# Kernel optimization log

Measured on AMD Instinct MI355X. Metric: run time of the kernel, lower is better.

## Reference

```python
import jax, jax.numpy as jnp
import numpy as np

B, S, ENC, DEC = 32, 4096, 512, 512

def setup_inputs() -> dict:
    key = jax.random.key(0)
    k1, k2, k3, k4 = jax.random.split(key, 4)
    encoder_outputs = jax.random.normal(k1, (B, S, ENC), dtype=jnp.float32)
    hidden = jax.random.normal(k2, (B, DEC), dtype=jnp.float32)
    # nn.Linear(enc+dec, 1): weight [1, enc+dec], bias [1]
    bound = 1.0 / np.sqrt(ENC + DEC)
    W = jax.random.uniform(k3, (1, ENC + DEC), minval=-bound, maxval=bound, dtype=jnp.float32)
    b = jax.random.uniform(k4, (1,), minval=-bound, maxval=bound, dtype=jnp.float32)
    return {"encoder_outputs": encoder_outputs, "hidden": hidden, "W": W, "b": b}

def reference(encoder_outputs, hidden, W, b):
    enc_dim = encoder_outputs.shape[-1]
    w_enc = W[0, :enc_dim]   # [enc]
    w_dec = W[0, enc_dim:]   # [dec]
    # energy = Linear(concat(enc, hidden_repeated)) == enc @ w_enc + hid @ w_dec + b
    energy = jnp.einsum('bse,e->bs', encoder_outputs, w_enc) \
           + (hidden @ w_dec)[:, None] + b[0]               # [B,S]
    weights = jax.nn.softmax(energy, axis=1)                 # [B,S]
    context = jnp.einsum('bs,bse->be', weights, encoder_outputs)  # [B,enc]
    return context
```

## Files before the change

### kernel.cpp

```cpp
#include <hip/hip_runtime.h>
#include <math.h>


#define B_ 32
#define S_ 4096
#define ENC_ 512
#define TPB 256
#define G 8

__device__ __forceinline__ float dot4(const float4 a, const float4 b) {
    return a.x * b.x + a.y * b.y + a.z * b.z + a.w * b.w;
}

__global__ __launch_bounds__(TPB) void attn_partial(
    const float* __restrict__ enc,
    const float* __restrict__ W,
    float* __restrict__ pm,
    float* __restrict__ pl,
    float* __restrict__ pc,
    int R, int P)
{
    const int b    = blockIdx.y;
    const int wid  = (blockIdx.x << 2) | (threadIdx.x >> 6);
    const int lane = threadIdx.x & 63;
    const int cA0  = lane << 2;
    const int cB0  = 256 + (lane << 2);

    const float4 wA = *reinterpret_cast<const float4*>(W + cA0);
    const float4 wB = *reinterpret_cast<const float4*>(W + cB0);

    const float* row = enc + ((size_t)b * S_ + (size_t)wid * R) * ENC_;

    float4 accA = {0.f, 0.f, 0.f, 0.f}, accB = {0.f, 0.f, 0.f, 0.f};
    float m = -INFINITY, l = 0.f;

    float4 dA0[G], dB0[G], dA1[G], dB1[G];

#define LOADG(DA, DB, base_row) { \
    const float* _p = row + (size_t)(base_row) * ENC_; \
    _Pragma("unroll") \
    for (int i = 0; i < G; ++i) { \
        DA[i] = *reinterpret_cast<const float4*>(_p + (size_t)i * ENC_ + cA0); \
        DB[i] = *reinterpret_cast<const float4*>(_p + (size_t)i * ENC_ + cB0); \
    } }

#define PROC(DA, DB) { \
    float e[G]; \
    _Pragma("unroll") \
    for (int i = 0; i < G; ++i) e[i] = dot4(DA[i], wA) + dot4(DB[i], wB); \
    _Pragma("unroll") \
    for (int i = 0; i < G; ++i) { \
        float v = e[i]; \
        v += __shfl_xor(v, 1, 64);  v += __shfl_xor(v, 2, 64); \
        v += __shfl_xor(v, 4, 64);  v += __shfl_xor(v, 8, 64); \
        v += __shfl_xor(v, 16, 64); v += __shfl_xor(v, 32, 64); \
        e[i] = v; \
    } \
    float gm = e[0]; \
    _Pragma("unroll") \
    for (int i = 1; i < G; ++i) gm = fmaxf(gm, e[i]); \
    const float mn = fmaxf(m, gm); \
    const float sc = __expf(m - mn);   \
    m = mn; l *= sc; \
    accA.x *= sc; accA.y *= sc; accA.z *= sc; accA.w *= sc; \
    accB.x *= sc; accB.y *= sc; accB.z *= sc; accB.w *= sc; \
    _Pragma("unroll") \
    for (int i = 0; i < G; ++i) { \
        const float pw = __expf(e[i] - mn); l += pw; \
        accA.x += pw * DA[i].x; accA.y += pw * DA[i].y; \
        accA.z += pw * DA[i].z; accA.w += pw * DA[i].w; \
        accB.x += pw * DB[i].x; accB.y += pw * DB[i].y; \
        accB.z += pw * DB[i].z; accB.w += pw * DB[i].w; \
    } }

    LOADG(dA0, dB0, 0);
    const int ng = R / G;
    for (int g = 0; g < ng; g += 2) {
        if (g + 1 < ng) LOADG(dA1, dB1, (g + 1) * G);
        PROC(dA0, dB0);
        if (g + 2 < ng) LOADG(dA0, dB0, (g + 2) * G);
        if (g + 1 < ng) PROC(dA1, dB1);
    }

    const int idx = b * P + wid;
    *reinterpret_cast<float4*>(pc + (size_t)idx * ENC_ + cA0) = accA;
    *reinterpret_cast<float4*>(pc + (size_t)idx * ENC_ + cB0) = accB;
    if (lane == 0) { pm[idx] = m; pl[idx] = l; }

#undef LOADG
#undef PROC
}

__global__ __launch_bounds__(TPB) void attn_combine(
    const float* __restrict__ pm, const float* __restrict__ pl,
    const float* __restrict__ pc, float* __restrict__ out, int P)
{
    const int b    = blockIdx.y;
    const int lane = threadIdx.x & 63;
    const int wave = threadIdx.x >> 6;
    const int col  = (blockIdx.x << 6) | lane;

    const float mv = (lane < P) ? pm[b * P + lane] : -INFINITY;
    float M = mv;
#pragma unroll
    for (int o = 32; o >= 1; o >>= 1) M = fmaxf(M, __shfl_xor(M, o, 64));
    const float sv = (lane < P) ? __expf(mv - M) : 0.f;
    float L = (lane < P) ? pl[b * P + lane] * sv : 0.f;
#pragma unroll
    for (int o = 32; o >= 1; o >>= 1) L += __shfl_xor(L, o, 64);

    const int per = P >> 2;
    float acc = 0.f;
    for (int k = 0; k < per; ++k) {
        const int i = wave * per + k;
        const float s = __shfl(sv, i, 64);
        acc += pc[((size_t)(b * P + i) << 9) | col] * s;
    }

    __shared__ float red[3][64];
    if (wave) red[wave - 1][lane] = acc;
    __syncthreads();
    if (wave == 0) {
        acc += red[0][lane] + red[1][lane] + red[2][lane];
        out[(b << 9) | col] = acc / L;
    }
}

extern "C" void kernel_launch(void* const* d_in, const int* in_sizes, int n_in,
                              void* d_out, int out_size, void* d_ws, size_t ws_size,
                              hipStream_t stream) {
    const float* enc = (const float*)d_in[0];
    const float* W   = (const float*)d_in[2];
    float* out       = (float*)d_out;

    int P = 64;
    while (P > 4 && (size_t)B_ * P * (ENC_ + 2) * sizeof(float) > ws_size) P >>= 1;
    const int R = S_ / P;

    float* pm = (float*)d_ws;
    float* pl = pm + (size_t)B_ * P;
    float* pc = pl + (size_t)B_ * P;

    dim3 grid1(P / 4, B_);
    attn_partial<<<grid1, TPB, 0, stream>>>(enc, W, pm, pl, pc, R, P);
    dim3 grid2(ENC_ / 64, B_);
    attn_combine<<<grid2, TPB, 0, stream>>>(pm, pl, pc, out, P);
}
```

Before: 55.32 us.

## Fuse partial and combine kernels via last-block atomic counter

Merges the two kernels into one: each block writes its partial softmax state, bumps a per-batch atomic counter, and the last block for each batch does the combine in-kernel. Loads of the encoder tensor become nontemporal, and the accumulation uses native vector types. This removes the second kernel launch and its inter-kernel gap, but adds a memset launch, fences, and a serialized tail in which one block per batch reads all partials.

```diff
diff --git a/kernel.cpp b/kernel.cpp
--- a/kernel.cpp
+++ b/kernel.cpp
@@ -8,40 +8,48 @@
 #define TPB 256
 #define G 8
 
-__device__ __forceinline__ float dot4(const float4 a, const float4 b) {
+typedef float f4 __attribute__((ext_vector_type(4)));
+
+__device__ __forceinline__ float dot4(const f4 a, const f4 b) {
     return a.x * b.x + a.y * b.y + a.z * b.z + a.w * b.w;
 }
 
-__global__ __launch_bounds__(TPB) void attn_partial(
+__global__ __launch_bounds__(TPB) void attn_fused(
     const float* __restrict__ enc,
     const float* __restrict__ W,
     float* __restrict__ pm,
     float* __restrict__ pl,
     float* __restrict__ pc,
+    int* __restrict__ counter,
+    float* __restrict__ out,
     int R, int P)
 {
     const int b    = blockIdx.y;
-    const int wid  = (blockIdx.x << 2) | (threadIdx.x >> 6);
-    const int lane = threadIdx.x & 63;
+    const int tid  = threadIdx.x;
+    const int wave = tid >> 6;
+    const int lane = tid & 63;
+    const int wid  = (blockIdx.x << 2) | wave;
     const int cA0  = lane << 2;
     const int cB0  = 256 + (lane << 2);
 
-    const float4 wA = *reinterpret_cast<const float4*>(W + cA0);
-    const float4 wB = *reinterpret_cast<const float4*>(W + cB0);
+    const f4 wA = *reinterpret_cast<const f4*>(W + cA0);
+    const f4 wB = *reinterpret_cast<const f4*>(W + cB0);
 
     const float* row = enc + ((size_t)b * S_ + (size_t)wid * R) * ENC_;
 
-    float4 accA = {0.f, 0.f, 0.f, 0.f}, accB = {0.f, 0.f, 0.f, 0.f};
+    f4 accA = {0.f, 0.f, 0.f, 0.f}, accB = {0.f, 0.f, 0.f, 0.f};
     float m = -INFINITY, l = 0.f;
 
-    float4 dA0[G], dB0[G], dA1[G], dB1[G];
+    f4 dA0[G], dB0[G], dA1[G], dB1[G];
 
 #define LOADG(DA, DB, base_row) { \
     const float* _p = row + (size_t)(base_row) * ENC_; \
     _Pragma("unroll") \
     for (int i = 0; i < G; ++i) { \
-        DA[i] = *reinterpret_cast<const float4*>(_p + (size_t)i * ENC_ + cA0); \
-        DB[i] = *reinterpret_cast<const float4*>(_p + (size_t)i * ENC_ + cB0); \
+        DA[i] = __builtin_nontemporal_load( \
+                    reinterpret_cast<const f4*>(_p + (size_t)i * ENC_ + cA0)); \
+        DB[i] = __builtin_nontemporal_load( \
+                    reinterpret_cast<const f4*>(_p + (size_t)i * ENC_ + cB0)); \
     } }
 
 #define PROC(DA, DB) { \
@@ -62,15 +70,12 @@
     const float mn = fmaxf(m, gm); \
     const float sc = __expf(m - mn);   \
     m = mn; l *= sc; \
-    accA.x *= sc; accA.y *= sc; accA.z *= sc; accA.w *= sc; \
-    accB.x *= sc; accB.y *= sc; accB.z *= sc; accB.w *= sc; \
+    accA *= sc; accB *= sc; \
     _Pragma("unroll") \
     for (int i = 0; i < G; ++i) { \
         const float pw = __expf(e[i] - mn); l += pw; \
-        accA.x += pw * DA[i].x; accA.y += pw * DA[i].y; \
-        accA.z += pw * DA[i].z; accA.w += pw * DA[i].w; \
-        accB.x += pw * DB[i].x; accB.y += pw * DB[i].y; \
-        accB.z += pw * DB[i].z; accB.w += pw * DB[i].w; \
+        accA += pw * DA[i]; \
+        accB += pw * DB[i]; \
     } }
 
     LOADG(dA0, dB0, 0);
@@ -83,22 +88,23 @@
     }
 
     const int idx = b * P + wid;
-    *reinterpret_cast<float4*>(pc + (size_t)idx * ENC_ + cA0) = accA;
-    *reinterpret_cast<float4*>(pc + (size_t)idx * ENC_ + cB0) = accB;
+    *reinterpret_cast<f4*>(pc + (size_t)idx * ENC_ + cA0) = accA;
+    *reinterpret_cast<f4*>(pc + (size_t)idx * ENC_ + cB0) = accB;
     if (lane == 0) { pm[idx] = m; pl[idx] = l; }
 
 #undef LOADG
 #undef PROC
-}
 
-__global__ __launch_bounds__(TPB) void attn_combine(
-    const float* __restrict__ pm, const float* __restrict__ pl,
-    const float* __restrict__ pc, float* __restrict__ out, int P)
-{
-    const int b    = blockIdx.y;
-    const int lane = threadIdx.x & 63;
-    const int wave = threadIdx.x >> 6;
-    const int col  = (blockIdx.x << 6) | lane;
+    __threadfence();
+    __syncthreads();
+    __shared__ int isLast;
+    if (tid == 0) {
+        const int v = atomicAdd(&counter[b], 1);
+        isLast = (v == (P >> 2) - 1);
+    }
+    __syncthreads();
+    if (!isLast) return;
+    __threadfence();
 
     const float mv = (lane < P) ? pm[b * P + lane] : -INFINITY;
     float M = mv;
@@ -109,21 +115,18 @@
 #pragma unroll
     for (int o = 32; o >= 1; o >>= 1) L += __shfl_xor(L, o, 64);
 
-    const int per = P >> 2;
-    float acc = 0.f;
-    for (int k = 0; k < per; ++k) {
-        const int i = wave * per + k;
-        const float s = __shfl(sv, i, 64);
-        acc += pc[((size_t)(b * P + i) << 9) | col] * s;
+    const int col = tid << 1;
+    float ax = 0.f, ay = 0.f;
+#pragma unroll 8
+    for (int i = 0; i < P; ++i) {
+        const float s = __shfl(sv, i & 63, 64);
+        const float2 v = *reinterpret_cast<const float2*>(
+            pc + ((size_t)(b * P + i) << 9) + col);
+        ax += v.x * s; ay += v.y * s;
     }
-
-    __shared__ float red[3][64];
-    if (wave) red[wave - 1][lane] = acc;
-    __syncthreads();
-    if (wave == 0) {
-        acc += red[0][lane] + red[1][lane] + red[2][lane];
-        out[(b << 9) | col] = acc / L;
-    }
+    const float inv = 1.f / L;
+    float2 o2; o2.x = ax * inv; o2.y = ay * inv;
+    *reinterpret_cast<float2*>(out + ((size_t)b << 9) + col) = o2;
 }
 
 extern "C" void kernel_launch(void* const* d_in, const int* in_sizes, int n_in,
@@ -134,15 +137,16 @@
     float* out       = (float*)d_out;
 
     int P = 64;
-    while (P > 4 && (size_t)B_ * P * (ENC_ + 2) * sizeof(float) > ws_size) P >>= 1;
+    while (P > 4 && 256 + (size_t)B_ * P * (ENC_ + 2) * sizeof(float) > ws_size) P >>= 1;
     const int R = S_ / P;
 
-    float* pm = (float*)d_ws;
+    int*   counter = (int*)d_ws;
+    float* pm = (float*)((char*)d_ws + 256);
     float* pl = pm + (size_t)B_ * P;
     float* pc = pl + (size_t)B_ * P;
 
-    dim3 grid1(P / 4, B_);
-    attn_partial<<<grid1, TPB, 0, stream>>>(enc, W, pm, pl, pc, R, P);
-    dim3 grid2(ENC_ / 64, B_);
-    attn_combine<<<grid2, TPB, 0, stream>>>(pm, pl, pc, out, P);
+    (void)hipMemsetAsync(counter, 0, B_ * sizeof(int), stream);
+
+    dim3 grid(P / 4, B_);
+    attn_fused<<<grid, TPB, 0, stream>>>(enc, W, pm, pl, pc, counter, out, R, P);
 }
```

Measured after the change: 185.9 us. +236.1%, slower.
